# Optimization experiments

Hardware: AMD Instinct MI355X
Metric: run time of the kernel (lower is better)

The kernel has to match this reference:

```python
import jax, jax.numpy as jnp
import numpy as np

H, D, HID = 16, 128, 2048
B, S = 2, 2048
NUM_BLOCKS, BLOCK_SIZE = 32, 128


def _rope(x, cos, sin):
    # x: [T, H, D]; cos/sin: [T, D/2] (neox / rotate-half style)
    half = x.shape[-1] // 2
    x1, x2 = x[..., :half], x[..., half:]
    c = cos[:, None, :]
    s = sin[:, None, :]
    return jnp.concatenate([x1 * c - x2 * s, x2 * c + x1 * s], axis=-1)


def setup_inputs() -> dict:
    key = jax.random.key(0)
    ks = jax.random.split(key, 6)
    T = B * S
    hidden_states = jax.random.normal(ks[0], (T, HID), jnp.float32)
    wqkv = jax.random.normal(ks[1], (HID, 3 * HID), jnp.float32) * 0.02
    bqkv = jax.random.normal(ks[2], (3 * HID,), jnp.float32) * 0.02
    wo = jax.random.normal(ks[3], (HID, HID), jnp.float32) * 0.02
    # rotary tables, base 10000, dim = head_size
    inv_freq = 1.0 / (10000.0 ** (jnp.arange(0, D, 2, dtype=jnp.float32) / D))  # [D/2]
    pos = jnp.tile(jnp.arange(S, dtype=jnp.float32), B)  # positions per token [T]
    ang = pos[:, None] * inv_freq[None, :]  # [T, D/2]
    cos, sin = jnp.cos(ang), jnp.sin(ang)
    k_cache = jnp.zeros((NUM_BLOCKS, BLOCK_SIZE, H, D), jnp.float32)
    v_cache = jnp.zeros((NUM_BLOCKS, BLOCK_SIZE, H, D), jnp.float32)
    cu_seqlen_prefill = jnp.array([0, S, 2 * S], jnp.int32)
    slots = jnp.arange(T, dtype=jnp.int32)
    return {"hidden_states": hidden_states, "cos": cos, "sin": sin,
            "wqkv": wqkv, "bqkv": bqkv, "wo": wo,
            "k_cache": k_cache, "v_cache": v_cache,
            "cu_seqlen_prefill": cu_seqlen_prefill, "slots": slots, "max_s": S}


def reference(hidden_states, cos, sin, wqkv, bqkv, wo, k_cache, v_cache,
              cu_seqlen_prefill, slots, max_s):
    T = hidden_states.shape[0]
    # fused QKV projection (c_attn)
    qkv = hidden_states @ wqkv + bqkv  # [T, 3*H*D]
    q, k, v = jnp.split(qkv, [H * D, 2 * H * D], axis=1)
    q = q.reshape(T, H, D)
    k = k.reshape(T, H, D)
    v = v.reshape(T, H, D)
    # rotary embedding on q and k (in-place in torch; functional here)
    q = _rope(q, cos, sin)
    k = _rope(k, cos, sin)
    # reshape_and_cache: scatter post-rope k and v into paged KV cache by slot
    kc = k_cache.reshape(-1, H, D).at[slots].set(k).reshape(k_cache.shape)
    vc = v_cache.reshape(-1, H, D).at[slots].set(v).reshape(v_cache.shape)
    # prefill flash attention: varlen causal; equal-length sequences here
    b, s = T // max_s, max_s
    qb = q.reshape(b, s, H, D)
    kb = k.reshape(b, s, H, D)
    vb = v.reshape(b, s, H, D)
    scale = D ** -0.5
    scores = jnp.einsum('bqhd,bkhd->bhqk', qb, kb) * scale  # [B,H,S,S]
    causal = jnp.tril(jnp.ones((s, s), bool))
    scores = jnp.where(causal[None, None], scores, jnp.finfo(scores.dtype).min)
    probs = jax.nn.softmax(scores, axis=-1)
    attn = jnp.einsum('bhqk,bkhd->bqhd', probs, vb).reshape(T, H * D)
    out = attn @ wo  # c_proj, no bias
    return out, kc, vc
```

## Files before the change

kernel.cpp:

```cpp
#include <hip/hip_runtime.h>

using f32x4  = __attribute__((ext_vector_type(4))) float;
using frag16 = __attribute__((ext_vector_type(8))) short;
using s16x4  = __attribute__((ext_vector_type(4))) short;
using s16x8  = __attribute__((ext_vector_type(8))) short;
using u32x4  = __attribute__((ext_vector_type(4))) unsigned;

#define DI __device__ __forceinline__

constexpr int HID  = 2048;
constexpr int NH   = 16;
constexpr int HD   = 128;
constexpr int TT   = 4096;
constexpr int SEQ  = 2048;
constexpr int NQKV = 3 * HID;

DI short f2bf(float f) {
  unsigned u = __builtin_bit_cast(unsigned, f);
  unsigned r = (u + 0x7fffu + ((u >> 16) & 1u)) >> 16;
  return (short)r;
}
DI float bf2f(short s) {
  unsigned u = ((unsigned)(unsigned short)s) << 16;
  return __builtin_bit_cast(float, u);
}
DI unsigned cvtpk(float lo, float hi) {
  unsigned r;
  asm("v_cvt_pk_bf16_f32 %0, %1, %2" : "=v"(r) : "v"(lo), "v"(hi));
  return r;
}

struct alignas(8) S4h { short a, b, c, d; };

__global__ void conv_f32_bf16(const float* __restrict__ in, short* __restrict__ out) {
  int gid = blockIdx.x * 256 + threadIdx.x;
  const float4* in4 = (const float4*)in;
  float4 v = in4[gid];
  S4h o{f2bf(v.x), f2bf(v.y), f2bf(v.z), f2bf(v.w)};
  ((S4h*)out)[gid] = o;
}

template <bool IN_F32, bool PERM>
__global__ void transpose_conv(const void* __restrict__ in_, short* __restrict__ out,
                               int ldin, int R) {
  __shared__ float t[64][65];
  const float* inf = (const float*)in_;
  const short* ins = (const short*)in_;
  int tid = threadIdx.x;
  int bx = blockIdx.x, by = blockIdx.y;
#pragma unroll
  for (int i = 0; i < 16; i++) {
    int idx = i * 256 + tid;
    int r = idx >> 6, c = idx & 63;
    size_t gi = (size_t)(by * 64 + r) * ldin + bx * 64 + c;
    t[r][c] = IN_F32 ? inf[gi] : bf2f(ins[gi]);
  }
  __syncthreads();
#pragma unroll
  for (int i = 0; i < 16; i++) {
    int idx = i * 256 + tid;
    int r = idx >> 6, c = idx & 63;
    int cs = PERM ? (16 * (c & 3) + 4 * (c >> 4) + ((c >> 2) & 3)) : c;
    out[(size_t)(bx * 64 + r) * R + by * 64 + c] = f2bf(t[cs][r]);
  }
}

#define GLDS(src, dst)                                                     \
  __builtin_amdgcn_global_load_lds(                                        \
      (const __attribute__((address_space(1))) void*)(src),                \
      (__attribute__((address_space(3))) void*)(dst), 16, 0, 0)

template <bool ADD_BIAS, bool OUT_BF16>
__global__ __launch_bounds__(256, 2) void gemm_bt(
    const short* __restrict__ A, const short* __restrict__ Bt,
    const float* __restrict__ bias, void* __restrict__ Cout,
    int M, int N, int K) {
  __shared__ alignas(16) short Al[128 * 64];
  __shared__ alignas(16) short Bl[128 * 64];
  const int tid = threadIdx.x;
  const int wid = tid >> 6, lane = tid & 63;
  const int wr = wid >> 1, wc = wid & 1;
  const int l15 = lane & 15, lg = lane >> 4;
  const int gx = gridDim.x;
  const int id = blockIdx.y * gx + blockIdx.x;
  const int nwg = gx * gridDim.y;
  const int swz = (id & 7) * (nwg >> 3) + (id >> 3);
  const int row0 = (swz / gx) * 128, col0 = (swz % gx) * 128;
  const int lr8 = lane >> 3, l7 = lane & 7;

  f32x4 acc[4][4];
#pragma unroll
  for (int i = 0; i < 4; i++)
#pragma unroll
    for (int j = 0; j < 4; j++) acc[i][j] = {0.f, 0.f, 0.f, 0.f};

  for (int kt = 0; kt < K; kt += 64) {
#pragma unroll
    for (int c = 0; c < 4; c++) {
      int chunk = c * 4 + wid;
      int r = chunk * 8 + lr8;
      int ke = (l7 * 8) ^ ((r & 7) * 8);
      GLDS(A + (size_t)(row0 + r) * K + kt + ke, Al + chunk * 512);
      GLDS(Bt + (size_t)(col0 + r) * K + kt + ke, Bl + chunk * 512);
    }
    __syncthreads();
#pragma unroll
    for (int kk = 0; kk < 2; kk++) {
      frag16 af[4], bfv[4];
#pragma unroll
      for (int ai = 0; ai < 4; ai++) {
        int r = wr * 64 + ai * 16 + l15;
        int k0 = kk * 32 + lg * 8;
        af[ai] = *(const frag16*)(Al + r * 64 + (k0 ^ ((r & 7) * 8)));
      }
#pragma unroll
      for (int bj = 0; bj < 4; bj++) {
        int r = wc * 64 + bj * 16 + l15;
        int k0 = kk * 32 + lg * 8;
        bfv[bj] = *(const frag16*)(Bl + r * 64 + (k0 ^ ((r & 7) * 8)));
      }
#pragma unroll
      for (int ai = 0; ai < 4; ai++)
#pragma unroll
        for (int bj = 0; bj < 4; bj++)
          acc[ai][bj] = __builtin_amdgcn_mfma_f32_16x16x32_bf16(
              af[ai], bfv[bj], acc[ai][bj], 0, 0, 0);
    }
    __syncthreads();
  }
#pragma unroll
  for (int ai = 0; ai < 4; ai++) {
#pragma unroll
    for (int bj = 0; bj < 4; bj++) {
      int row = row0 + wr * 64 + ai * 16 + lg * 4;
      int col = col0 + wc * 64 + bj * 16 + l15;
      float bv = 0.f;
      if (ADD_BIAS) bv = bias[col];
#pragma unroll
      for (int r = 0; r < 4; r++) {
        float v = acc[ai][bj][r] + bv;
        if (OUT_BF16)
          ((short*)Cout)[(size_t)(row + r) * N + col] = f2bf(v);
        else
          ((float*)Cout)[(size_t)(row + r) * N + col] = v;
      }
    }
  }
}

__global__ void rope_scatter(const short* __restrict__ qkv, const float* __restrict__ cs,
                             const float* __restrict__ sn, const int* __restrict__ slots,
                             short* __restrict__ Qb, short* __restrict__ Kb,
                             float* __restrict__ kc, float* __restrict__ vc) {
  const float SCL = 0.08838834764831845f * 1.4426950408889634f;
  const int t = blockIdx.x;
  const int tid = threadIdx.x;
  const int slot = slots[t];
  const short* row = qkv + (size_t)t * NQKV;
  short* qo = Qb + (size_t)t * HID;
  short* ko = Kb + (size_t)t * HID;
  float* kco = kc + (size_t)slot * HID;
  float* vco = vc + (size_t)slot * HID;

  const int h = tid >> 4, d0 = (tid & 15) * 4;
  const int c1 = h * 128 + d0, c2 = c1 + 64;
  float4 c4 = *(const float4*)(cs + (size_t)t * 64 + d0);
  float4 s4 = *(const float4*)(sn + (size_t)t * 64 + d0);
  float cc[4] = {c4.x, c4.y, c4.z, c4.w};
  float ssv[4] = {s4.x, s4.y, s4.z, s4.w};
  s16x4 q1 = *(const s16x4*)(row + c1);
  s16x4 q2 = *(const s16x4*)(row + c2);
  s16x4 k1 = *(const s16x4*)(row + HID + c1);
  s16x4 k2 = *(const s16x4*)(row + HID + c2);
  s16x4 qo1, qo2, ko1, ko2;
  float kcv1[4], kcv2[4];
#pragma unroll
  for (int r = 0; r < 4; r++) {
    float a = bf2f(q1[r]), b = bf2f(q2[r]);
    qo1[r] = f2bf((a * cc[r] - b * ssv[r]) * SCL);
    qo2[r] = f2bf((b * cc[r] + a * ssv[r]) * SCL);
    float ka = bf2f(k1[r]), kb = bf2f(k2[r]);
    float o1 = ka * cc[r] - kb * ssv[r];
    float o2 = kb * cc[r] + ka * ssv[r];
    ko1[r] = f2bf(o1);
    ko2[r] = f2bf(o2);
    kcv1[r] = o1;
    kcv2[r] = o2;
  }
  *(s16x4*)(qo + c1) = qo1;
  *(s16x4*)(qo + c2) = qo2;
  *(s16x4*)(ko + c1) = ko1;
  *(s16x4*)(ko + c2) = ko2;
  *(float4*)(kco + c1) = {kcv1[0], kcv1[1], kcv1[2], kcv1[3]};
  *(float4*)(kco + c2) = {kcv2[0], kcv2[1], kcv2[2], kcv2[3]};

  const int vi = tid * 8;
  s16x8 v8 = *(const s16x8*)(row + 2 * HID + vi);
  *(float4*)(vco + vi)     = {bf2f(v8[0]), bf2f(v8[1]), bf2f(v8[2]), bf2f(v8[3])};
  *(float4*)(vco + vi + 4) = {bf2f(v8[4]), bf2f(v8[5]), bf2f(v8[6]), bf2f(v8[7])};
}

__global__ __launch_bounds__(256, 2) void flash_attn4(
    const short* __restrict__ Qb, const short* __restrict__ Kb,
    const short* __restrict__ Vt, short* __restrict__ attn) {
  __shared__ alignas(16) short Klds[2][64 * 128];
  __shared__ alignas(16) short Vlds[2][128 * 64];
  __shared__ alignas(16) short plds[4][16 * 72];

  const int tid = threadIdx.x;
  const int w = tid >> 6, lane = tid & 63;
  const int l15 = lane & 15, lg = lane >> 4;
  const int bid = blockIdx.x;
  const int pr = bid >> 5;
  const int bh = bid & 31;
  const int b = bh >> 4, h = bh & 15;
  short* pl = &plds[w][0];

  frag16 ones;
#pragma unroll
  for (int j = 0; j < 8; j++) ones[j] = (short)0x3F80;

  auto stage = [&](int kv0, int buf) {
#pragma unroll
    for (int ci = 0; ci < 4; ci++) {
      int cc = w * 4 + ci;
      int krow = cc * 4 + (lane >> 4);
      int ksp = lane & 15;
      int kss = ksp ^ (krow & 15);
      GLDS(Kb + (size_t)(b * SEQ + kv0 + krow) * HID + h * HD + kss * 8,
           Klds[buf] + cc * 512);
      int vd = cc * 8 + (lane >> 3);
      int vsp = lane & 7;
      int vss = vsp ^ (vd & 7);
      GLDS(Vt + (size_t)(h * HD + vd) * TT + b * SEQ + kv0 + vss * 8,
           Vlds[buf] + cc * 512);
    }
  };

  const int strips[2] = {31 - pr, pr};
#pragma unroll 1
  for (int spi = 0; spi < 2; spi++) {
    const int s = strips[spi];
    const int qrow0 = s * 64 + w * 16;
    const int nt = s + 1;

    frag16 qf[4];
    {
      const short* qp = Qb + (size_t)(b * SEQ + qrow0 + l15) * HID + h * HD + lg * 8;
#pragma unroll
      for (int ds = 0; ds < 4; ds++) qf[ds] = *(const frag16*)(qp + ds * 32);
    }
    f32x4 o[8];
#pragma unroll
    for (int j = 0; j < 8; j++) o[j] = {0.f, 0.f, 0.f, 0.f};
    f32x4 la = {0.f, 0.f, 0.f, 0.f};
    float mr = -1e30f;

    stage(0, 0);
    __syncthreads();

    int cur = 0;
    for (int t = 0; t < nt; t++) {
      const int kv0 = t * 64;
      if (t + 1 < nt) stage(kv0 + 64, cur ^ 1);

      const short* Kl = &Klds[cur][0];
      const short* Vl = &Vlds[cur][0];
      f32x4 sa[4];
#pragma unroll
      for (int f = 0; f < 4; f++) sa[f] = {0.f, 0.f, 0.f, 0.f};
#pragma unroll
      for (int ds = 0; ds < 4; ds++) {
        int phys = (ds * 4 + lg) ^ l15;
#pragma unroll
        for (int f = 0; f < 4; f++) {
          frag16 kf = *(const frag16*)(Kl + (f * 16 + l15) * 128 + phys * 8);
          sa[f] = __builtin_amdgcn_mfma_f32_16x16x32_bf16(kf, qf[ds], sa[f], 0, 0, 0);
        }
      }
      if (kv0 + 63 > qrow0) {
        int ql = 16 * w + l15;
#pragma unroll
        for (int f = 0; f < 4; f++)
#pragma unroll
          for (int r = 0; r < 4; r++)
            if (f * 16 + lg * 4 + r > ql) sa[f][r] = -1e30f;
      }
      float pm = sa[0][0];
#pragma unroll
      for (int f = 0; f < 4; f++)
#pragma unroll
        for (int r = 0; r < 4; r++) pm = fmaxf(pm, sa[f][r]);
      pm = fmaxf(pm, __shfl_xor(pm, 16));
      pm = fmaxf(pm, __shfl_xor(pm, 32));
      if (__any(pm > mr + 8.f)) {
        float mn = fmaxf(mr, pm);
        float frl = exp2f(mr - mn);
        mr = mn;
        float fr4[4];
#pragma unroll
        for (int r = 0; r < 4; r++)
          fr4[r] = __shfl(frl, lg * 16 + lg * 4 + r);
#pragma unroll
        for (int r = 0; r < 4; r++) {
          la[r] *= fr4[r];
#pragma unroll
          for (int j = 0; j < 8; j++) o[j][r] *= fr4[r];
        }
      }
      float pe[4][4];
#pragma unroll
      for (int f = 0; f < 4; f++)
#pragma unroll
        for (int r = 0; r < 4; r++) pe[f][r] = exp2f(sa[f][r] - mr);
      unsigned wv[8];
#pragma unroll
      for (int r = 0; r < 4; r++) {
        wv[2 * r]     = cvtpk(pe[0][r], pe[1][r]);
        wv[2 * r + 1] = cvtpk(pe[2][r], pe[3][r]);
      }
      {
        u32x4* pb = (u32x4*)(pl + l15 * 72 + lg * 16);
        pb[0] = {wv[0], wv[1], wv[2], wv[3]};
        pb[1] = {wv[4], wv[5], wv[6], wv[7]};
      }
      asm volatile("s_waitcnt lgkmcnt(0)" ::: "memory");
      frag16 pf0 = *(const frag16*)(pl + l15 * 72 + lg * 8);
      frag16 pf1 = *(const frag16*)(pl + l15 * 72 + 32 + lg * 8);
      la = __builtin_amdgcn_mfma_f32_16x16x32_bf16(pf0, ones, la, 0, 0, 0);
      la = __builtin_amdgcn_mfma_f32_16x16x32_bf16(pf1, ones, la, 0, 0, 0);
#pragma unroll
      for (int j = 0; j < 8; j++) {
        int d = j * 16 + l15;
        int p0 = lg ^ (d & 7);
        int p1 = (4 + lg) ^ (d & 7);
        frag16 vf0 = *(const frag16*)(Vl + d * 64 + p0 * 8);
        frag16 vf1 = *(const frag16*)(Vl + d * 64 + p1 * 8);
        o[j] = __builtin_amdgcn_mfma_f32_16x16x32_bf16(pf0, vf0, o[j], 0, 0, 0);
        o[j] = __builtin_amdgcn_mfma_f32_16x16x32_bf16(pf1, vf1, o[j], 0, 0, 0);
      }
      __syncthreads();
      cur ^= 1;
    }

    float inv[4];
#pragma unroll
    for (int r = 0; r < 4; r++) inv[r] = 1.f / la[r];
    short* op = attn + (size_t)(b * SEQ + qrow0 + lg * 4) * HID + h * HD + l15;
#pragma unroll
    for (int j = 0; j < 8; j++)
#pragma unroll
      for (int r = 0; r < 4; r++)
        op[(size_t)r * HID + j * 16] = f2bf(o[j][r] * inv[r]);
  }
}

extern "C" void kernel_launch(void* const* d_in, const int* in_sizes, int n_in,
                              void* d_out, int out_size, void* d_ws, size_t ws_size,
                              hipStream_t stream) {
  const float* hidden = (const float*)d_in[0];
  const float* cosb   = (const float*)d_in[1];
  const float* sinb   = (const float*)d_in[2];
  const float* wqkv   = (const float*)d_in[3];
  const float* bqkv   = (const float*)d_in[4];
  const float* wo     = (const float*)d_in[5];
  const int*   slots  = (const int*)d_in[9];

  float* out = (float*)d_out;
  float* kc  = out + (size_t)TT * HID;
  float* vc  = kc + (size_t)TT * HID;

  short* ws    = (short*)d_ws;
  short* Abf   = ws;
  short* Wqkvt = Abf + 8388608;
  short* Wot   = Wqkvt + 12582912;
  short* qkvb  = Wot + 4194304;
  short* Qb    = qkvb + 25165824;
  short* Kb    = Qb + 8388608;
  short* Vt    = Kb + 8388608;
  short* attnb = Abf;

  conv_f32_bf16<<<8192, 256, 0, stream>>>(hidden, Abf);
  transpose_conv<true, false><<<dim3(96, 32), 256, 0, stream>>>(wqkv, Wqkvt, NQKV, HID);
  transpose_conv<true, false><<<dim3(32, 32), 256, 0, stream>>>(wo, Wot, HID, HID);
  gemm_bt<true, true><<<dim3(48, 32), 256, 0, stream>>>(Abf, Wqkvt, bqkv, qkvb,
                                                        TT, NQKV, HID);
  rope_scatter<<<TT, 256, 0, stream>>>(qkvb, cosb, sinb, slots, Qb, Kb, kc, vc);
  transpose_conv<false, true><<<dim3(32, 64), 256, 0, stream>>>(qkvb + 2 * HID, Vt, NQKV, TT);
  flash_attn4<<<512, 256, 0, stream>>>(Qb, Kb, Vt, attnb);
  gemm_bt<false, false><<<dim3(16, 32), 256, 0, stream>>>(attnb, Wot, nullptr, out,
                                                          TT, HID, HID);
}
```

Measured before the change: 297.9 us.

## Replace GEMM with 256x128 tile, double-buffered LDS and interleaved prefetch

Replaces the 128x128 single-buffered GEMM with a 256x128-tile, 512-thread kernel. LDS is double-buffered and the next K tile's global-to-LDS loads are split across four compute phases, using manual vmcnt waits, raw barriers and setprio around the MFMA blocks. The goal is to hide global load latency behind MFMA work and raise reuse per block. The cost is higher LDS use (96KB per block), fewer blocks for the output projection (256 blocks), and fragile hand-written synchronization.

```diff
diff --git a/kernel.cpp b/kernel.cpp
--- a/kernel.cpp
+++ b/kernel.cpp
@@ -70,75 +70,169 @@
       (const __attribute__((address_space(1))) void*)(src),                \
       (__attribute__((address_space(3))) void*)(dst), 16, 0, 0)
 
+#define WAITVM2 asm volatile("s_waitcnt vmcnt(2)" ::: "memory")
+#define WAITVM0 asm volatile("s_waitcnt vmcnt(0)" ::: "memory")
+#define BARRIER asm volatile("s_barrier" ::: "memory")
+
 template <bool ADD_BIAS, bool OUT_BF16>
-__global__ __launch_bounds__(256, 2) void gemm_bt(
+__global__ __launch_bounds__(512, 2) void gemm_bt256(
     const short* __restrict__ A, const short* __restrict__ Bt,
     const float* __restrict__ bias, void* __restrict__ Cout,
     int M, int N, int K) {
-  __shared__ alignas(16) short Al[128 * 64];
-  __shared__ alignas(16) short Bl[128 * 64];
+  __shared__ alignas(16) short Al[2][256 * 64];
+  __shared__ alignas(16) short Bl[2][128 * 64];
   const int tid = threadIdx.x;
   const int wid = tid >> 6, lane = tid & 63;
-  const int wr = wid >> 1, wc = wid & 1;
+  const int wrm = wid >> 2, wcn = wid & 3;
   const int l15 = lane & 15, lg = lane >> 4;
   const int gx = gridDim.x;
   const int id = blockIdx.y * gx + blockIdx.x;
   const int nwg = gx * gridDim.y;
   const int swz = (id & 7) * (nwg >> 3) + (id >> 3);
-  const int row0 = (swz / gx) * 128, col0 = (swz % gx) * 128;
-  const int lr8 = lane >> 3, l7 = lane & 7;
-
-  f32x4 acc[4][4];
-#pragma unroll
-  for (int i = 0; i < 4; i++)
-#pragma unroll
-    for (int j = 0; j < 4; j++) acc[i][j] = {0.f, 0.f, 0.f, 0.f};
-
-  for (int kt = 0; kt < K; kt += 64) {
-#pragma unroll
-    for (int c = 0; c < 4; c++) {
-      int chunk = c * 4 + wid;
-      int r = chunk * 8 + lr8;
-      int ke = (l7 * 8) ^ ((r & 7) * 8);
-      GLDS(A + (size_t)(row0 + r) * K + kt + ke, Al + chunk * 512);
-      GLDS(Bt + (size_t)(col0 + r) * K + kt + ke, Bl + chunk * 512);
-    }
-    __syncthreads();
-#pragma unroll
-    for (int kk = 0; kk < 2; kk++) {
-      frag16 af[4], bfv[4];
-#pragma unroll
-      for (int ai = 0; ai < 4; ai++) {
-        int r = wr * 64 + ai * 16 + l15;
-        int k0 = kk * 32 + lg * 8;
-        af[ai] = *(const frag16*)(Al + r * 64 + (k0 ^ ((r & 7) * 8)));
-      }
-#pragma unroll
-      for (int bj = 0; bj < 4; bj++) {
-        int r = wc * 64 + bj * 16 + l15;
-        int k0 = kk * 32 + lg * 8;
-        bfv[bj] = *(const frag16*)(Bl + r * 64 + (k0 ^ ((r & 7) * 8)));
-      }
-#pragma unroll
-      for (int ai = 0; ai < 4; ai++)
-#pragma unroll
-        for (int bj = 0; bj < 4; bj++)
-          acc[ai][bj] = __builtin_amdgcn_mfma_f32_16x16x32_bf16(
-              af[ai], bfv[bj], acc[ai][bj], 0, 0, 0);
-    }
-    __syncthreads();
-  }
-#pragma unroll
-  for (int ai = 0; ai < 4; ai++) {
-#pragma unroll
-    for (int bj = 0; bj < 4; bj++) {
-      int row = row0 + wr * 64 + ai * 16 + lg * 4;
-      int col = col0 + wc * 64 + bj * 16 + l15;
+  const int row0 = (swz / gx) * 256, col0 = (swz % gx) * 128;
+
+  f32x4 acc[8][2];
+#pragma unroll
+  for (int i = 0; i < 8; i++)
+#pragma unroll
+    for (int j = 0; j < 2; j++) acc[i][j] = {0.f, 0.f, 0.f, 0.f};
+
+  auto stageA = [&](int kt, int buf, int g) {
+    int idx = g * 512 + tid;
+    int row = idx >> 3;
+    int ke = ((idx & 7) ^ (row & 7)) * 8;
+    GLDS(A + (size_t)(row0 + row) * K + kt + ke,
+         &Al[buf][0] + (size_t)(g * 512 + wid * 64) * 8);
+  };
+  auto stageB = [&](int kt, int buf, int g) {
+    int idx = g * 512 + tid;
+    int row = idx >> 3;
+    int ke = ((idx & 7) ^ (row & 7)) * 8;
+    GLDS(Bt + (size_t)(col0 + row) * K + kt + ke,
+         &Bl[buf][0] + (size_t)(g * 512 + wid * 64) * 8);
+  };
+
+  const int NT = K >> 6;
+#pragma unroll
+  for (int g = 0; g < 4; g++) stageA(0, 0, g);
+#pragma unroll
+  for (int g = 0; g < 2; g++) stageB(0, 0, g);
+
+  for (int t = 0; t < NT; ++t) {
+    const int buf = t & 1;
+    const int ktn = (t + 1) << 6;
+    const bool pf = (t + 1 < NT);
+
+    if (pf) { stageA(ktn, buf ^ 1, 0); stageA(ktn, buf ^ 1, 1); WAITVM2; }
+    else    { WAITVM0; }
+    BARRIER;
+    frag16 bfr[2][2];
+#pragma unroll
+    for (int ct = 0; ct < 2; ct++)
+#pragma unroll
+      for (int kk = 0; kk < 2; kk++) {
+        int rb = wcn * 32 + ct * 16 + l15;
+        bfr[ct][kk] = *(const frag16*)(&Bl[buf][rb * 64 + (((kk * 4 + lg) ^ (rb & 7)) * 8)]);
+      }
+    {
+      frag16 af[2][2];
+#pragma unroll
+      for (int r2 = 0; r2 < 2; r2++)
+#pragma unroll
+        for (int kk = 0; kk < 2; kk++) {
+          int ra = wrm * 128 + (0 + r2) * 16 + l15;
+          af[r2][kk] = *(const frag16*)(&Al[buf][ra * 64 + (((kk * 4 + lg) ^ (ra & 7)) * 8)]);
+        }
+      __builtin_amdgcn_s_setprio(1);
+#pragma unroll
+      for (int r2 = 0; r2 < 2; r2++)
+#pragma unroll
+        for (int ct = 0; ct < 2; ct++)
+#pragma unroll
+          for (int kk = 0; kk < 2; kk++)
+            acc[0 + r2][ct] = __builtin_amdgcn_mfma_f32_16x16x32_bf16(
+                af[r2][kk], bfr[ct][kk], acc[0 + r2][ct], 0, 0, 0);
+      __builtin_amdgcn_s_setprio(0);
+    }
+    BARRIER;
+    if (pf) { stageA(ktn, buf ^ 1, 2); stageA(ktn, buf ^ 1, 3); }
+    {
+      frag16 af[2][2];
+#pragma unroll
+      for (int r2 = 0; r2 < 2; r2++)
+#pragma unroll
+        for (int kk = 0; kk < 2; kk++) {
+          int ra = wrm * 128 + (2 + r2) * 16 + l15;
+          af[r2][kk] = *(const frag16*)(&Al[buf][ra * 64 + (((kk * 4 + lg) ^ (ra & 7)) * 8)]);
+        }
+      __builtin_amdgcn_s_setprio(1);
+#pragma unroll
+      for (int r2 = 0; r2 < 2; r2++)
+#pragma unroll
+        for (int ct = 0; ct < 2; ct++)
+#pragma unroll
+          for (int kk = 0; kk < 2; kk++)
+            acc[2 + r2][ct] = __builtin_amdgcn_mfma_f32_16x16x32_bf16(
+                af[r2][kk], bfr[ct][kk], acc[2 + r2][ct], 0, 0, 0);
+      __builtin_amdgcn_s_setprio(0);
+    }
+    BARRIER;
+    if (pf) { stageB(ktn, buf ^ 1, 0); stageB(ktn, buf ^ 1, 1); }
+    {
+      frag16 af[2][2];
+#pragma unroll
+      for (int r2 = 0; r2 < 2; r2++)
+#pragma unroll
+        for (int kk = 0; kk < 2; kk++) {
+          int ra = wrm * 128 + (4 + r2) * 16 + l15;
+          af[r2][kk] = *(const frag16*)(&Al[buf][ra * 64 + (((kk * 4 + lg) ^ (ra & 7)) * 8)]);
+        }
+      __builtin_amdgcn_s_setprio(1);
+#pragma unroll
+      for (int r2 = 0; r2 < 2; r2++)
+#pragma unroll
+        for (int ct = 0; ct < 2; ct++)
+#pragma unroll
+          for (int kk = 0; kk < 2; kk++)
+            acc[4 + r2][ct] = __builtin_amdgcn_mfma_f32_16x16x32_bf16(
+                af[r2][kk], bfr[ct][kk], acc[4 + r2][ct], 0, 0, 0);
+      __builtin_amdgcn_s_setprio(0);
+    }
+    BARRIER;
+    {
+      frag16 af[2][2];
+#pragma unroll
+      for (int r2 = 0; r2 < 2; r2++)
+#pragma unroll
+        for (int kk = 0; kk < 2; kk++) {
+          int ra = wrm * 128 + (6 + r2) * 16 + l15;
+          af[r2][kk] = *(const frag16*)(&Al[buf][ra * 64 + (((kk * 4 + lg) ^ (ra & 7)) * 8)]);
+        }
+      __builtin_amdgcn_s_setprio(1);
+#pragma unroll
+      for (int r2 = 0; r2 < 2; r2++)
+#pragma unroll
+        for (int ct = 0; ct < 2; ct++)
+#pragma unroll
+          for (int kk = 0; kk < 2; kk++)
+            acc[6 + r2][ct] = __builtin_amdgcn_mfma_f32_16x16x32_bf16(
+                af[r2][kk], bfr[ct][kk], acc[6 + r2][ct], 0, 0, 0);
+      __builtin_amdgcn_s_setprio(0);
+    }
+    BARRIER;
+  }
+
+#pragma unroll
+  for (int rt = 0; rt < 8; rt++) {
+#pragma unroll
+    for (int ct = 0; ct < 2; ct++) {
+      int row = row0 + wrm * 128 + rt * 16 + lg * 4;
+      int col = col0 + wcn * 32 + ct * 16 + l15;
       float bv = 0.f;
       if (ADD_BIAS) bv = bias[col];
 #pragma unroll
       for (int r = 0; r < 4; r++) {
-        float v = acc[ai][bj][r] + bv;
+        float v = acc[rt][ct][r] + bv;
         if (OUT_BF16)
           ((short*)Cout)[(size_t)(row + r) * N + col] = f2bf(v);
         else
@@ -383,11 +477,11 @@
   conv_f32_bf16<<<8192, 256, 0, stream>>>(hidden, Abf);
   transpose_conv<true, false><<<dim3(96, 32), 256, 0, stream>>>(wqkv, Wqkvt, NQKV, HID);
   transpose_conv<true, false><<<dim3(32, 32), 256, 0, stream>>>(wo, Wot, HID, HID);
-  gemm_bt<true, true><<<dim3(48, 32), 256, 0, stream>>>(Abf, Wqkvt, bqkv, qkvb,
-                                                        TT, NQKV, HID);
+  gemm_bt256<true, true><<<dim3(48, 16), 512, 0, stream>>>(Abf, Wqkvt, bqkv, qkvb,
+                                                           TT, NQKV, HID);
   rope_scatter<<<TT, 256, 0, stream>>>(qkvb, cosb, sinb, slots, Qb, Kb, kc, vc);
   transpose_conv<false, true><<<dim3(32, 64), 256, 0, stream>>>(qkvb + 2 * HID, Vt, NQKV, TT);
   flash_attn4<<<512, 256, 0, stream>>>(Qb, Kb, Vt, attnb);
-  gemm_bt<false, false><<<dim3(16, 32), 256, 0, stream>>>(attnb, Wot, nullptr, out,
-                                                          TT, HID, HID);
-}
+  gemm_bt256<false, false><<<dim3(16, 16), 512, 0, stream>>>(attnb, Wot, nullptr, out,
+                                                             TT, HID, HID);
+}
```

After: 409.7 us. 37.5% more time.

## Share K/V tiles between paired causal strips and vectorize transpose kernels

Applied to the files above, without the earlier changes.

The attention kernel used to process its two paired query strips one after the other, staging K/V tiles for each. It now keeps both strips' accumulators live and processes them together over a single K/V pass, so the low strip reuses tiles already staged for the high strip. This removes about half of the K/V global-to-LDS traffic and barriers, but doubles the accumulator register state, which could cause spills or lower occupancy under launch_bounds(256,2). Separately, the transpose/convert kernels now use 4-wide vector loads and stores in place of scalar accesses.

```diff
diff --git a/kernel.cpp b/kernel.cpp
--- a/kernel.cpp
+++ b/kernel.cpp
@@ -49,19 +49,33 @@
   int tid = threadIdx.x;
   int bx = blockIdx.x, by = blockIdx.y;
 #pragma unroll
-  for (int i = 0; i < 16; i++) {
+  for (int i = 0; i < 4; i++) {
     int idx = i * 256 + tid;
-    int r = idx >> 6, c = idx & 63;
-    size_t gi = (size_t)(by * 64 + r) * ldin + bx * 64 + c;
-    t[r][c] = IN_F32 ? inf[gi] : bf2f(ins[gi]);
+    int r = idx >> 4, c4 = idx & 15;
+    size_t gi = (size_t)(by * 64 + r) * ldin + bx * 64 + c4 * 4;
+    if (IN_F32) {
+      float4 v = *(const float4*)(inf + gi);
+      t[r][c4 * 4] = v.x; t[r][c4 * 4 + 1] = v.y;
+      t[r][c4 * 4 + 2] = v.z; t[r][c4 * 4 + 3] = v.w;
+    } else {
+      s16x4 v = *(const s16x4*)(ins + gi);
+#pragma unroll
+      for (int j = 0; j < 4; j++) t[r][c4 * 4 + j] = bf2f(v[j]);
+    }
   }
   __syncthreads();
 #pragma unroll
-  for (int i = 0; i < 16; i++) {
+  for (int i = 0; i < 4; i++) {
     int idx = i * 256 + tid;
-    int r = idx >> 6, c = idx & 63;
-    int cs = PERM ? (16 * (c & 3) + 4 * (c >> 4) + ((c >> 2) & 3)) : c;
-    out[(size_t)(bx * 64 + r) * R + by * 64 + c] = f2bf(t[cs][r]);
+    int r = idx >> 4, c4 = idx & 15;
+    s16x4 o;
+#pragma unroll
+    for (int j = 0; j < 4; j++) {
+      int c = c4 * 4 + j;
+      int cs = PERM ? (16 * (c & 3) + 4 * (c >> 4) + ((c >> 2) & 3)) : c;
+      o[j] = f2bf(t[cs][r]);
+    }
+    *(s16x4*)(out + (size_t)(bx * 64 + r) * R + by * 64 + c4 * 4) = o;
   }
 }
 
@@ -200,7 +214,7 @@
   *(float4*)(vco + vi + 4) = {bf2f(v8[4]), bf2f(v8[5]), bf2f(v8[6]), bf2f(v8[7])};
 }
 
-__global__ __launch_bounds__(256, 2) void flash_attn4(
+__global__ __launch_bounds__(256, 2) void flash_attn5(
     const short* __restrict__ Qb, const short* __restrict__ Kb,
     const short* __restrict__ Vt, short* __restrict__ attn) {
   __shared__ alignas(16) short Klds[2][64 * 128];
@@ -211,7 +225,7 @@
   const int w = tid >> 6, lane = tid & 63;
   const int l15 = lane & 15, lg = lane >> 4;
   const int bid = blockIdx.x;
-  const int pr = bid >> 5;
+  const int p = bid >> 5;
   const int bh = bid & 31;
   const int b = bh >> 4, h = bh & 15;
   short* pl = &plds[w][0];
@@ -225,133 +239,148 @@
     for (int ci = 0; ci < 4; ci++) {
       int cc = w * 4 + ci;
       int krow = cc * 4 + (lane >> 4);
-      int ksp = lane & 15;
-      int kss = ksp ^ (krow & 15);
+      int kss = (lane & 15) ^ (krow & 15);
       GLDS(Kb + (size_t)(b * SEQ + kv0 + krow) * HID + h * HD + kss * 8,
            Klds[buf] + cc * 512);
       int vd = cc * 8 + (lane >> 3);
-      int vsp = lane & 7;
-      int vss = vsp ^ (vd & 7);
+      int vss = (lane & 7) ^ (vd & 7);
       GLDS(Vt + (size_t)(h * HD + vd) * TT + b * SEQ + kv0 + vss * 8,
            Vlds[buf] + cc * 512);
     }
   };
 
-  const int strips[2] = {31 - pr, pr};
-#pragma unroll 1
-  for (int spi = 0; spi < 2; spi++) {
-    const int s = strips[spi];
-    const int qrow0 = s * 64 + w * 16;
-    const int nt = s + 1;
-
-    frag16 qf[4];
+  const int qrowH = (31 - p) * 64 + w * 16;
+  const int qrowL = p * 64 + w * 16;
+  const int ntH = 32 - p;
+
+  frag16 qfH[4], qfL[4];
+  {
+    const short* qpH = Qb + (size_t)(b * SEQ + qrowH + l15) * HID + h * HD + lg * 8;
+    const short* qpL = Qb + (size_t)(b * SEQ + qrowL + l15) * HID + h * HD + lg * 8;
+#pragma unroll
+    for (int ds = 0; ds < 4; ds++) {
+      qfH[ds] = *(const frag16*)(qpH + ds * 32);
+      qfL[ds] = *(const frag16*)(qpL + ds * 32);
+    }
+  }
+  f32x4 oH[8], oL[8];
+#pragma unroll
+  for (int j = 0; j < 8; j++) { oH[j] = {0.f, 0.f, 0.f, 0.f}; oL[j] = {0.f, 0.f, 0.f, 0.f}; }
+  f32x4 laH = {0.f, 0.f, 0.f, 0.f}, laL = {0.f, 0.f, 0.f, 0.f};
+  float mrH = -1e30f, mrL = -1e30f;
+
+  auto proc = [&](const frag16 (&qf)[4], f32x4 (&o)[8], f32x4& la, float& mr,
+                  bool diag, const short* Kl, const short* Vl) {
+    f32x4 sa[4];
+#pragma unroll
+    for (int f = 0; f < 4; f++) sa[f] = {0.f, 0.f, 0.f, 0.f};
+#pragma unroll
+    for (int ds = 0; ds < 4; ds++) {
+      int phys = (ds * 4 + lg) ^ l15;
+#pragma unroll
+      for (int f = 0; f < 4; f++) {
+        frag16 kf = *(const frag16*)(Kl + (f * 16 + l15) * 128 + phys * 8);
+        sa[f] = __builtin_amdgcn_mfma_f32_16x16x32_bf16(kf, qf[ds], sa[f], 0, 0, 0);
+      }
+    }
+    if (diag) {
+      int ql = 16 * w + l15;
+#pragma unroll
+      for (int f = 0; f < 4; f++)
+#pragma unroll
+        for (int r = 0; r < 4; r++)
+          if (f * 16 + lg * 4 + r > ql) sa[f][r] = -1e30f;
+    }
+    float pm = sa[0][0];
+#pragma unroll
+    for (int f = 0; f < 4; f++)
+#pragma unroll
+      for (int r = 0; r < 4; r++) pm = fmaxf(pm, sa[f][r]);
+    pm = fmaxf(pm, __shfl_xor(pm, 16));
+    pm = fmaxf(pm, __shfl_xor(pm, 32));
+    if (__any(pm > mr + 8.f)) {
+      float mn = fmaxf(mr, pm);
+      float frl = exp2f(mr - mn);
+      mr = mn;
+      float fr4[4];
+#pragma unroll
+      for (int r = 0; r < 4; r++)
+        fr4[r] = __shfl(frl, lg * 16 + lg * 4 + r);
+#pragma unroll
+      for (int r = 0; r < 4; r++) {
+        la[r] *= fr4[r];
+#pragma unroll
+        for (int j = 0; j < 8; j++) o[j][r] *= fr4[r];
+      }
+    }
+    float pe[4][4];
+#pragma unroll
+    for (int f = 0; f < 4; f++)
+#pragma unroll
+      for (int r = 0; r < 4; r++) pe[f][r] = exp2f(sa[f][r] - mr);
+    unsigned wv[8];
+#pragma unroll
+    for (int r = 0; r < 4; r++) {
+      wv[2 * r]     = cvtpk(pe[0][r], pe[1][r]);
+      wv[2 * r + 1] = cvtpk(pe[2][r], pe[3][r]);
+    }
     {
-      const short* qp = Qb + (size_t)(b * SEQ + qrow0 + l15) * HID + h * HD + lg * 8;
-#pragma unroll
-      for (int ds = 0; ds < 4; ds++) qf[ds] = *(const frag16*)(qp + ds * 32);
-    }
-    f32x4 o[8];
-#pragma unroll
-    for (int j = 0; j < 8; j++) o[j] = {0.f, 0.f, 0.f, 0.f};
-    f32x4 la = {0.f, 0.f, 0.f, 0.f};
-    float mr = -1e30f;
-
-    stage(0, 0);
+      u32x4* pb = (u32x4*)(pl + l15 * 72 + lg * 16);
+      pb[0] = {wv[0], wv[1], wv[2], wv[3]};
+      pb[1] = {wv[4], wv[5], wv[6], wv[7]};
+    }
+    asm volatile("s_waitcnt lgkmcnt(0)" ::: "memory");
+    frag16 pf0 = *(const frag16*)(pl + l15 * 72 + lg * 8);
+    frag16 pf1 = *(const frag16*)(pl + l15 * 72 + 32 + lg * 8);
+    la = __builtin_amdgcn_mfma_f32_16x16x32_bf16(pf0, ones, la, 0, 0, 0);
+    la = __builtin_amdgcn_mfma_f32_16x16x32_bf16(pf1, ones, la, 0, 0, 0);
+#pragma unroll
+    for (int j = 0; j < 8; j++) {
+      int d = j * 16 + l15;
+      int p0 = lg ^ (d & 7);
+      int p1 = (4 + lg) ^ (d & 7);
+      frag16 vf0 = *(const frag16*)(Vl + d * 64 + p0 * 8);
+      frag16 vf1 = *(const frag16*)(Vl + d * 64 + p1 * 8);
+      o[j] = __builtin_amdgcn_mfma_f32_16x16x32_bf16(pf0, vf0, o[j], 0, 0, 0);
+      o[j] = __builtin_amdgcn_mfma_f32_16x16x32_bf16(pf1, vf1, o[j], 0, 0, 0);
+    }
+  };
+
+  stage(0, 0);
+  __syncthreads();
+
+  int cur = 0;
+  for (int t = 0; t < ntH; t++) {
+    if (t + 1 < ntH) stage((t + 1) * 64, cur ^ 1);
+    const short* Kl = &Klds[cur][0];
+    const short* Vl = &Vlds[cur][0];
+    proc(qfH, oH, laH, mrH, t == ntH - 1, Kl, Vl);
+    if (t <= p) proc(qfL, oL, laL, mrL, t == p, Kl, Vl);
     __syncthreads();
-
-    int cur = 0;
-    for (int t = 0; t < nt; t++) {
-      const int kv0 = t * 64;
-      if (t + 1 < nt) stage(kv0 + 64, cur ^ 1);
-
-      const short* Kl = &Klds[cur][0];
-      const short* Vl = &Vlds[cur][0];
-      f32x4 sa[4];
-#pragma unroll
-      for (int f = 0; f < 4; f++) sa[f] = {0.f, 0.f, 0.f, 0.f};
-#pragma unroll
-      for (int ds = 0; ds < 4; ds++) {
-        int phys = (ds * 4 + lg) ^ l15;
-#pragma unroll
-        for (int f = 0; f < 4; f++) {
-          frag16 kf = *(const frag16*)(Kl + (f * 16 + l15) * 128 + phys * 8);
-          sa[f] = __builtin_amdgcn_mfma_f32_16x16x32_bf16(kf, qf[ds], sa[f], 0, 0, 0);
-        }
-      }
-      if (kv0 + 63 > qrow0) {
-        int ql = 16 * w + l15;
-#pragma unroll
-        for (int f = 0; f < 4; f++)
-#pragma unroll
-          for (int r = 0; r < 4; r++)
-            if (f * 16 + lg * 4 + r > ql) sa[f][r] = -1e30f;
-      }
-      float pm = sa[0][0];
-#pragma unroll
-      for (int f = 0; f < 4; f++)
-#pragma unroll
-        for (int r = 0; r < 4; r++) pm = fmaxf(pm, sa[f][r]);
-      pm = fmaxf(pm, __shfl_xor(pm, 16));
-      pm = fmaxf(pm, __shfl_xor(pm, 32));
-      if (__any(pm > mr + 8.f)) {
-        float mn = fmaxf(mr, pm);
-        float frl = exp2f(mr - mn);
-        mr = mn;
-        float fr4[4];
-#pragma unroll
-        for (int r = 0; r < 4; r++)
-          fr4[r] = __shfl(frl, lg * 16 + lg * 4 + r);
-#pragma unroll
-        for (int r = 0; r < 4; r++) {
-          la[r] *= fr4[r];
-#pragma unroll
-          for (int j = 0; j < 8; j++) o[j][r] *= fr4[r];
-        }
-      }
-      float pe[4][4];
-#pragma unroll
-      for (int f = 0; f < 4; f++)
-#pragma unroll
-        for (int r = 0; r < 4; r++) pe[f][r] = exp2f(sa[f][r] - mr);
-      unsigned wv[8];
-#pragma unroll
-      for (int r = 0; r < 4; r++) {
-        wv[2 * r]     = cvtpk(pe[0][r], pe[1][r]);
-        wv[2 * r + 1] = cvtpk(pe[2][r], pe[3][r]);
-      }
-      {
-        u32x4* pb = (u32x4*)(pl + l15 * 72 + lg * 16);
-        pb[0] = {wv[0], wv[1], wv[2], wv[3]};
-        pb[1] = {wv[4], wv[5], wv[6], wv[7]};
-      }
-      asm volatile("s_waitcnt lgkmcnt(0)" ::: "memory");
-      frag16 pf0 = *(const frag16*)(pl + l15 * 72 + lg * 8);
-      frag16 pf1 = *(const frag16*)(pl + l15 * 72 + 32 + lg * 8);
-      la = __builtin_amdgcn_mfma_f32_16x16x32_bf16(pf0, ones, la, 0, 0, 0);
-      la = __builtin_amdgcn_mfma_f32_16x16x32_bf16(pf1, ones, la, 0, 0, 0);
-#pragma unroll
-      for (int j = 0; j < 8; j++) {
-        int d = j * 16 + l15;
-        int p0 = lg ^ (d & 7);
-        int p1 = (4 + lg) ^ (d & 7);
-        frag16 vf0 = *(const frag16*)(Vl + d * 64 + p0 * 8);
-        frag16 vf1 = *(const frag16*)(Vl + d * 64 + p1 * 8);
-        o[j] = __builtin_amdgcn_mfma_f32_16x16x32_bf16(pf0, vf0, o[j], 0, 0, 0);
-        o[j] = __builtin_amdgcn_mfma_f32_16x16x32_bf16(pf1, vf1, o[j], 0, 0, 0);
-      }
-      __syncthreads();
-      cur ^= 1;
-    }
-
+    cur ^= 1;
+  }
+
+  {
     float inv[4];
 #pragma unroll
-    for (int r = 0; r < 4; r++) inv[r] = 1.f / la[r];
-    short* op = attn + (size_t)(b * SEQ + qrow0 + lg * 4) * HID + h * HD + l15;
+    for (int r = 0; r < 4; r++) inv[r] = 1.f / laH[r];
+    short* op = attn + (size_t)(b * SEQ + qrowH + lg * 4) * HID + h * HD + l15;
 #pragma unroll
     for (int j = 0; j < 8; j++)
 #pragma unroll
       for (int r = 0; r < 4; r++)
-        op[(size_t)r * HID + j * 16] = f2bf(o[j][r] * inv[r]);
+        op[(size_t)r * HID + j * 16] = f2bf(oH[j][r] * inv[r]);
+  }
+  {
+    float inv[4];
+#pragma unroll
+    for (int r = 0; r < 4; r++) inv[r] = 1.f / laL[r];
+    short* op = attn + (size_t)(b * SEQ + qrowL + lg * 4) * HID + h * HD + l15;
+#pragma unroll
+    for (int j = 0; j < 8; j++)
+#pragma unroll
+      for (int r = 0; r < 4; r++)
+        op[(size_t)r * HID + j * 16] = f2bf(oL[j][r] * inv[r]);
   }
 }
 
@@ -387,7 +416,7 @@
                                                         TT, NQKV, HID);
   rope_scatter<<<TT, 256, 0, stream>>>(qkvb, cosb, sinb, slots, Qb, Kb, kc, vc);
   transpose_conv<false, true><<<dim3(32, 64), 256, 0, stream>>>(qkvb + 2 * HID, Vt, NQKV, TT);
-  flash_attn4<<<512, 256, 0, stream>>>(Qb, Kb, Vt, attnb);
+  flash_attn5<<<512, 256, 0, stream>>>(Qb, Kb, Vt, attnb);
   gemm_bt<false, false><<<dim3(16, 32), 256, 0, stream>>>(attnb, Wot, nullptr, out,
                                                           TT, HID, HID);
 }
```

Measured after the change: 291.8 us. 2.0% less time.
